# Performance work log

Measured on AMD Instinct MI355X. Metric: run time of the kernel, lower is better.

The kernel has to match this reference:

```python
import math
import jax, jax.numpy as jnp
import numpy as np

B, S, H = 4, 4096, 1024
NH, HD = 16, 64
MLP_DIM = 4096


def _gelu_tanh(x):
    c = math.sqrt(2.0 / math.pi)
    return 0.5 * x * (1.0 + jnp.tanh(c * (x + 0.044715 * x * x * x)))


def _layernorm(x, w, b, eps=1e-5):
    mu = jnp.mean(x, axis=-1, keepdims=True)
    var = jnp.var(x, axis=-1, keepdims=True)
    return (x - mu) * jax.lax.rsqrt(var + eps) * w + b


def setup_inputs() -> dict:
    key = jax.random.key(0)
    ks = jax.random.split(key, 12)
    s = 0.02
    return {
        "x": jax.random.normal(ks[0], (B, S, H), jnp.float32),
        "ln1_w": jnp.ones((H,), jnp.float32),
        "ln1_b": jnp.zeros((H,), jnp.float32),
        "q_w": jax.random.normal(ks[1], (H, H), jnp.float32) * s,
        "q_b": jnp.zeros((H,), jnp.float32),
        "k_w": jax.random.normal(ks[2], (H, H), jnp.float32) * s,
        "k_b": jnp.zeros((H,), jnp.float32),
        "v_w": jax.random.normal(ks[3], (H, H), jnp.float32) * s,
        "v_b": jnp.zeros((H,), jnp.float32),
        "o_w": jax.random.normal(ks[4], (H, H), jnp.float32) * s,
        "o_b": jnp.zeros((H,), jnp.float32),
        "ln2_w": jnp.ones((H,), jnp.float32),
        "ln2_b": jnp.zeros((H,), jnp.float32),
        "fc_w": jax.random.normal(ks[5], (H, MLP_DIM), jnp.float32) * s,
        "fc_b": jnp.zeros((MLP_DIM,), jnp.float32),
        "proj_w": jax.random.normal(ks[6], (MLP_DIM, H), jnp.float32) * (s / math.sqrt(2 * 12)),
        "proj_b": jnp.zeros((H,), jnp.float32),
    }


def reference(x, ln1_w, ln1_b, q_w, q_b, k_w, k_b, v_w, v_b, o_w, o_b,
              ln2_w, ln2_b, fc_w, fc_b, proj_w, proj_b):
    bsz, seqlen, h = x.shape
    ln_x = _layernorm(x, ln1_w, ln1_b)

    # projections -> [b, nh, t, hd]
    def heads(y):
        return y.reshape(bsz, seqlen, NH, HD).transpose(0, 2, 1, 3)

    q = heads(ln_x @ q_w + q_b)
    k = heads(ln_x @ k_w + k_b)
    v = heads(ln_x @ v_w + v_b)

    # feature map: elu(x)+1
    qf = jax.nn.elu(q) + 1.0
    kf = jax.nn.elu(k) + 1.0

    kv = jnp.einsum('bhtd,bhte->bhde', kf, v)              # [b,nh,hd,hd]
    norm = 1.0 / (jnp.einsum('bhtd,bhd->bht', qf, kf.sum(axis=2)) + 1e-6)
    out = jnp.einsum('bhtd,bhde->bhte', qf, kv) * norm[..., None]
    out = out.transpose(0, 2, 1, 3).reshape(bsz, seqlen, h)
    attn = out @ o_w + o_b

    x = x + attn
    h_mlp = _gelu_tanh(_layernorm(x, ln2_w, ln2_b) @ fc_w + fc_b)
    x = x + (h_mlp @ proj_w + proj_b)
    return x
```

## Files before the change

### kernel.cpp

```cpp
#include <hip/hip_runtime.h>
#include <hip/hip_bf16.h>
#include <cstdint>
#include <cstddef>

typedef __bf16 bf16;
typedef __bf16 bf16x8 __attribute__((ext_vector_type(8)));
typedef __bf16 bf16x4 __attribute__((ext_vector_type(4)));
typedef float  f32x4  __attribute__((ext_vector_type(4)));

typedef __attribute__((address_space(1))) void gvoid_t;
typedef __attribute__((address_space(3))) void lvoid_t;

#define GLD_LDS16(g, l) __builtin_amdgcn_global_load_lds( \
    (gvoid_t*)(uintptr_t)(g), (lvoid_t*)(uint32_t)(uintptr_t)(l), 16, 0, 0)

#define SBAR() __builtin_amdgcn_s_barrier()
#define SCHED_FENCE() __builtin_amdgcn_sched_barrier(0)
#define WAIT_VMN(n) asm volatile("s_waitcnt vmcnt(" #n ")" ::: "memory")
#define WAIT_LGKM0() asm volatile("s_waitcnt lgkmcnt(0)" ::: "memory")

__global__ __launch_bounds__(256) void transpose4(
    const float* __restrict__ qw, const float* __restrict__ kw,
    const float* __restrict__ vw, const float* __restrict__ ow,
    bf16* __restrict__ wqkvT, bf16* __restrict__ woT)
{
  __shared__ float tile[32][33];
  const int z = blockIdx.z;
  const float* in = z == 0 ? qw : (z == 1 ? kw : (z == 2 ? vw : ow));
  bf16* out = z == 3 ? woT : (wqkvT + (size_t)z * 1024 * 1024);
  const int bx = blockIdx.x, by = blockIdx.y;
  const int tx = threadIdx.x, ty = threadIdx.y;
#pragma unroll
  for (int i = 0; i < 32; i += 8)
    tile[ty + i][tx] = in[(size_t)(by * 32 + ty + i) * 1024 + bx * 32 + tx];
  __syncthreads();
#pragma unroll
  for (int i = 0; i < 32; i += 8)
    out[(size_t)(bx * 32 + ty + i) * 1024 + by * 32 + tx] = (bf16)tile[tx][ty + i];
}

__global__ __launch_bounds__(256) void transpose_cast(
    const float* __restrict__ in, bf16* __restrict__ out, int R, int C)
{
  __shared__ float tile[32][33];
  const int bx = blockIdx.x, by = blockIdx.y;
  const int tx = threadIdx.x, ty = threadIdx.y;
#pragma unroll
  for (int i = 0; i < 32; i += 8)
    tile[ty + i][tx] = in[(size_t)(by * 32 + ty + i) * C + bx * 32 + tx];
  __syncthreads();
#pragma unroll
  for (int i = 0; i < 32; i += 8)
    out[(size_t)(bx * 32 + ty + i) * R + by * 32 + tx] = (bf16)tile[tx][ty + i];
}

__global__ __launch_bounds__(256) void pack3(
    const float* __restrict__ a, const float* __restrict__ b,
    const float* __restrict__ c, float* __restrict__ o)
{
  const int i = blockIdx.x * 256 + threadIdx.x;
  o[i] = i < 1024 ? a[i] : (i < 2048 ? b[i - 1024] : c[i - 2048]);
}

__global__ __launch_bounds__(256) void ln_row(
    const float* __restrict__ x, const float* __restrict__ w,
    const float* __restrict__ b, bf16* __restrict__ out)
{
  const int row = blockIdx.x;
  const int tid = threadIdx.x;
  const float4 v = ((const float4*)(x + (size_t)row * 1024))[tid];
  float s  = v.x + v.y + v.z + v.w;
  float ss = v.x * v.x + v.y * v.y + v.z * v.z + v.w * v.w;
#pragma unroll
  for (int off = 32; off > 0; off >>= 1) {
    s  += __shfl_down(s, off);
    ss += __shfl_down(ss, off);
  }
  __shared__ float red[8];
  const int wid = tid >> 6, lane = tid & 63;
  if (lane == 0) { red[wid] = s; red[4 + wid] = ss; }
  __syncthreads();
  s  = red[0] + red[1] + red[2] + red[3];
  ss = red[4] + red[5] + red[6] + red[7];
  const float mu   = s * (1.f / 1024.f);
  const float var  = ss * (1.f / 1024.f) - mu * mu;
  const float rstd = rsqrtf(var + 1e-5f);
  const float4 wv = ((const float4*)w)[tid];
  const float4 bv = ((const float4*)b)[tid];
  bf16x4 ov;
  ov[0] = (bf16)((v.x - mu) * rstd * wv.x + bv.x);
  ov[1] = (bf16)((v.y - mu) * rstd * wv.y + bv.y);
  ov[2] = (bf16)((v.z - mu) * rstd * wv.z + bv.z);
  ov[3] = (bf16)((v.w - mu) * rstd * wv.w + bv.w);
  *(bf16x4*)(out + (size_t)row * 1024 + tid * 4) = ov;
}

template <int EPI>
__global__ __launch_bounds__(512, 2) void gemm256(
    const bf16* __restrict__ A, const bf16* __restrict__ BT,
    const float* __restrict__ bias, const float* __restrict__ resid,
    void* __restrict__ outp, int M, int N, int K, int nx)
{
  __shared__ __align__(16) char lds[131072];
  const int tid  = threadIdx.x;
  const int wid  = tid >> 6, lane = tid & 63;
  const int wr   = wid >> 2, wc = wid & 3;
  const int ln15 = lane & 15, lhi = lane >> 4;

  const int nwg = (int)gridDim.x;
  const int cpx = nwg >> 3;
  const int bid = (int)blockIdx.x;
  const int lg  = (bid & 7) * cpx + (bid >> 3);
  const int bx  = lg % nx, by = lg / nx;
  const int row0 = by << 8, col0 = bx << 8;

  const int srowA = tid >> 3;
  const int sslA  = (tid & 7) ^ (srowA & 7);
  const bf16* aS  = A + (size_t)(row0 + srowA) * K + sslA * 8;
  const size_t rjK = (size_t)K << 6;
  const int u8    = tid >> 3, s8 = tid & 7;
  const int gRowB = ((u8 >> 5) << 6) + (u8 & 31);
  const int sslB  = s8 ^ (u8 & 7);
  const bf16* bS  = BT + (size_t)(col0 + gRowB) * K + sslB * 8;

  char* ldsAw = lds + wid * 1024;
  char* ldsBw = lds + 65536 + wid * 1024;

  const int slk0 = (lhi ^ (ln15 & 7)) << 4;
  const int slk1 = ((4 + lhi) ^ (ln15 & 7)) << 4;
  const int rowA0 = ((wr << 7) + ln15) * 128;
  const int rowB0 = 65536 + (wc * 32 + ln15) * 128;

  f32x4 acc[8][4] = {};
  bf16x8 a[4][2], b0[2][2], b1[2][2];
  const int nt = K >> 6;

#define STG_A(D, KT, I) GLD_LDS16(aS + (size_t)(I) * rjK + (size_t)(KT) * 64, \
                                  ldsAw + (D) * 32768 + (I) * 8192)
#define STG_B(D, KT, NH, J) GLD_LDS16(bS + (size_t)((J) * 128 + (NH) * 32) * K + (size_t)(KT) * 64, \
                                      ldsBw + (D) * 32768 + (NH) * 16384 + (J) * 8192)
#define RD_A(D, MH) do { _Pragma("unroll") \
    for (int m_ = 0; m_ < 4; ++m_) { \
      a[m_][0] = *(const bf16x8*)(lds + (D) * 32768 + rowA0 + (MH) * 8192 + m_ * 2048 + slk0); \
      a[m_][1] = *(const bf16x8*)(lds + (D) * 32768 + rowA0 + (MH) * 8192 + m_ * 2048 + slk1); \
    } } while (0)
#define RD_B(D, NH, DST) do { _Pragma("unroll") \
    for (int n_ = 0; n_ < 2; ++n_) { \
      DST[n_][0] = *(const bf16x8*)(lds + (D) * 32768 + rowB0 + (NH) * 16384 + n_ * 2048 + slk0); \
      DST[n_][1] = *(const bf16x8*)(lds + (D) * 32768 + rowB0 + (NH) * 16384 + n_ * 2048 + slk1); \
    } } while (0)
#define MFMA8(MH, NH, BSRC) do { \
    __builtin_amdgcn_s_setprio(1); \
    _Pragma("unroll") for (int m_ = 0; m_ < 4; ++m_) \
    _Pragma("unroll") for (int n_ = 0; n_ < 2; ++n_) { \
      acc[(MH) * 4 + m_][(NH) * 2 + n_] = __builtin_amdgcn_mfma_f32_16x16x32_bf16( \
          a[m_][0], BSRC[n_][0], acc[(MH) * 4 + m_][(NH) * 2 + n_], 0, 0, 0); \
      acc[(MH) * 4 + m_][(NH) * 2 + n_] = __builtin_amdgcn_mfma_f32_16x16x32_bf16( \
          a[m_][1], BSRC[n_][1], acc[(MH) * 4 + m_][(NH) * 2 + n_], 0, 0, 0); \
    } \
    __builtin_amdgcn_s_setprio(0); } while (0)

  STG_A(0, 0, 0); STG_A(0, 0, 2);
  STG_B(0, 0, 0, 0); STG_B(0, 0, 0, 1);
  STG_B(0, 0, 1, 0); STG_B(0, 0, 1, 1);
  STG_A(0, 0, 1); STG_A(0, 0, 3);
  WAIT_VMN(0);
  SBAR(); SCHED_FENCE();

  for (int kt = 0; kt < nt - 1; ++kt) {
    const int d = kt & 1, dn = d ^ 1;
    RD_A(d, 0); RD_B(d, 0, b0);
    STG_A(dn, kt + 1, 0); STG_A(dn, kt + 1, 2);
    SBAR(); WAIT_LGKM0(); SCHED_FENCE();
    MFMA8(0, 0, b0);
    SBAR(); SCHED_FENCE();
    RD_B(d, 1, b1);
    STG_B(dn, kt + 1, 0, 0); STG_B(dn, kt + 1, 0, 1);
    WAIT_VMN(4);
    SBAR(); WAIT_LGKM0(); SCHED_FENCE();
    MFMA8(0, 1, b1);
    SBAR(); SCHED_FENCE();
    RD_A(d, 1);
    STG_B(dn, kt + 1, 1, 0); STG_B(dn, kt + 1, 1, 1);
    SBAR(); WAIT_LGKM0(); SCHED_FENCE();
    MFMA8(1, 0, b0);
    SBAR(); SCHED_FENCE();
    STG_A(dn, kt + 1, 1); STG_A(dn, kt + 1, 3);
    MFMA8(1, 1, b1);
    WAIT_VMN(2);
    SBAR(); SCHED_FENCE();
  }

  {
    const int d = (nt - 1) & 1;
    RD_A(d, 0); RD_B(d, 0, b0);
    SBAR(); WAIT_LGKM0(); SCHED_FENCE();
    MFMA8(0, 0, b0);
    SBAR(); SCHED_FENCE();
    RD_B(d, 1, b1);
    WAIT_VMN(0);
    SBAR(); WAIT_LGKM0(); SCHED_FENCE();
    MFMA8(0, 1, b1);
    SBAR(); SCHED_FENCE();
    RD_A(d, 1);
    WAIT_LGKM0(); SCHED_FENCE();
    MFMA8(1, 0, b0);
    MFMA8(1, 1, b1);
  }
#undef STG_A
#undef STG_B
#undef RD_A
#undef RD_B
#undef MFMA8

  const int lr4 = lhi << 2;
#pragma unroll
  for (int m = 0; m < 8; ++m) {
#pragma unroll
    for (int n = 0; n < 4; ++n) {
      const int c_i = col0 + wc * 64 + n * 16 + ln15;
      const float bv = bias[c_i];
#pragma unroll
      for (int j = 0; j < 4; ++j) {
        const int r_i = row0 + wr * 128 + m * 16 + lr4 + j;
        const size_t idx = (size_t)r_i * N + c_i;
        float val = acc[m][n][j] + bv;
        if constexpr (EPI == 0) {
          ((bf16*)outp)[idx] = (bf16)val;
        } else if constexpr (EPI == 1) {
          ((bf16*)outp)[idx] = (bf16)(val > 0.f ? val + 1.f : __expf(val));
        } else if constexpr (EPI == 2) {
          ((float*)outp)[idx] = val + resid[idx];
        } else if constexpr (EPI == 3) {
          const float u  = 0.7978845608028654f * (val + 0.044715f * val * val * val);
          const float th = 1.f - 2.f / (__expf(2.f * u) + 1.f);
          ((bf16*)outp)[idx] = (bf16)(0.5f * val * (1.f + th));
        } else {
          if (c_i < 2048)
            ((bf16*)outp)[idx] = (bf16)(val > 0.f ? val + 1.f : __expf(val));
          else
            ((bf16*)outp)[idx] = (bf16)val;
        }
      }
    }
  }
}

__global__ __launch_bounds__(256) void kv_part_kernel(
    const bf16* __restrict__ qkv, float* __restrict__ kv_part,
    float* __restrict__ ksum_part)
{
  const int bh = blockIdx.x >> 3, ch = blockIdx.x & 7;
  const int b = bh >> 4, h = bh & 15;
  const int tid = threadIdx.x;
  const int d = tid & 63, eg = tid >> 6;
  const size_t grow0 = (size_t)b * 4096 + (size_t)ch * 512;
  const size_t vbase = 2048 + (size_t)h * 64;
  __shared__ bf16 svv[8][64], skf[8][64];
  float accum[16];
#pragma unroll
  for (int i = 0; i < 16; ++i) accum[i] = 0.f;
  float ks = 0.f;
  const int tt = tid >> 5, cc = (tid & 31) << 1;
  for (int t0 = 0; t0 < 512; t0 += 8) {
    __syncthreads();
    const size_t base = (grow0 + t0 + tt) * 3072 + vbase + cc;
    *(uint32_t*)&svv[tt][cc] = *(const uint32_t*)(qkv + base);
    *(uint32_t*)&skf[tt][cc] = *(const uint32_t*)(qkv + base - 1024);
    __syncthreads();
#pragma unroll
    for (int q = 0; q < 8; ++q) {
      const float kd = (float)skf[q][d];
      const uint32_t* u0 = (const uint32_t*)&svv[q][eg * 16];
#pragma unroll
      for (int i = 0; i < 8; ++i) {
        const uint32_t u = u0[i];
        const float lo = __uint_as_float(u << 16);
        const float hi = __uint_as_float(u & 0xffff0000u);
        accum[2 * i]     += lo * kd;
        accum[2 * i + 1] += hi * kd;
      }
    }
    if (tid < 64) {
#pragma unroll
      for (int q = 0; q < 8; ++q) ks += (float)skf[q][tid];
    }
  }
  float* op = kv_part + (size_t)blockIdx.x * 4096 + (size_t)(eg * 16) * 64 + d;
#pragma unroll
  for (int ee = 0; ee < 16; ++ee) op[ee * 64] = accum[ee];
  if (tid < 64) ksum_part[(size_t)blockIdx.x * 64 + tid] = ks;
}

__global__ __launch_bounds__(256) void kv_reduce(
    const float* __restrict__ kvp, const float* __restrict__ ksp,
    bf16* __restrict__ kb)
{
  const int bh = blockIdx.x;
  const int tid = threadIdx.x;
  bf16* KB = kb + (size_t)bh * 5120;
  for (int i = tid; i < 4096; i += 256) {
    float s = 0.f;
#pragma unroll
    for (int ch = 0; ch < 8; ++ch) s += kvp[((size_t)bh * 8 + ch) * 4096 + i];
    KB[i] = (bf16)s;
  }
  if (tid < 64) {
    float s = 0.f;
#pragma unroll
    for (int ch = 0; ch < 8; ++ch) s += ksp[((size_t)bh * 8 + ch) * 64 + tid];
    KB[4096 + tid] = (bf16)s;
  }
  for (int i = 4160 + tid; i < 5120; i += 256) KB[i] = (bf16)0.f;
}

__global__ __launch_bounds__(256) void attn_mfma(
    const bf16* __restrict__ qkv, const bf16* __restrict__ kb,
    bf16* __restrict__ attn)
{
  const int bh = blockIdx.x >> 4, rb = blockIdx.x & 15;
  const int b = bh >> 4, h = bh & 15;
  const int tid = threadIdx.x, wid = tid >> 6, lane = tid & 63;
  const int ln15 = lane & 15, lhi = lane >> 4;
  const size_t row0 = (size_t)b * 4096 + rb * 256 + wid * 64;
  const bf16* KB = kb + (size_t)bh * 5120;

  bf16x8 bfr[5][2];
#pragma unroll
  for (int nb = 0; nb < 5; ++nb)
#pragma unroll
    for (int ks = 0; ks < 2; ++ks)
      bfr[nb][ks] = *(const bf16x8*)(KB + (nb * 16 + ln15) * 64 + ks * 32 + lhi * 8);

  for (int mt = 0; mt < 4; ++mt) {
    const bf16* ap = qkv + (row0 + mt * 16 + ln15) * 3072 + h * 64 + lhi * 8;
    const bf16x8 a0 = *(const bf16x8*)ap;
    const bf16x8 a1 = *(const bf16x8*)(ap + 32);
    f32x4 acc[5];
#pragma unroll
    for (int nb = 0; nb < 5; ++nb) {
      f32x4 z = {0.f, 0.f, 0.f, 0.f};
      z = __builtin_amdgcn_mfma_f32_16x16x32_bf16(a0, bfr[nb][0], z, 0, 0, 0);
      acc[nb] = __builtin_amdgcn_mfma_f32_16x16x32_bf16(a1, bfr[nb][1], z, 0, 0, 0);
    }
#pragma unroll
    for (int j = 0; j < 4; ++j) {
      const float ns = __shfl(acc[4][j], (lane & 48));
      const float inv = 1.f / (ns + 1e-6f);
      const size_t r = row0 + mt * 16 + (lhi << 2) + j;
#pragma unroll
      for (int nb = 0; nb < 4; ++nb)
        attn[r * 1024 + h * 64 + nb * 16 + ln15] = (bf16)(acc[nb][j] * inv);
    }
  }
}

extern "C" void kernel_launch(void* const* d_in, const int* in_sizes, int n_in,
                              void* d_out, int out_size, void* d_ws, size_t ws_size,
                              hipStream_t stream)
{
  const float* x    = (const float*)d_in[0];
  const float* ln1w = (const float*)d_in[1];
  const float* ln1b = (const float*)d_in[2];
  const float* qw   = (const float*)d_in[3];
  const float* qb   = (const float*)d_in[4];
  const float* kw   = (const float*)d_in[5];
  const float* kb_  = (const float*)d_in[6];
  const float* vw   = (const float*)d_in[7];
  const float* vb   = (const float*)d_in[8];
  const float* ow   = (const float*)d_in[9];
  const float* ob   = (const float*)d_in[10];
  const float* ln2w = (const float*)d_in[11];
  const float* ln2b = (const float*)d_in[12];
  const float* fcw  = (const float*)d_in[13];
  const float* fcb  = (const float*)d_in[14];
  const float* pjw  = (const float*)d_in[15];
  const float* pjb  = (const float*)d_in[16];
  float* out = (float*)d_out;
  char* ws = (char*)d_ws;

  constexpr size_t O_LNX  = 0;
  constexpr size_t O_QKV  = 33554432;
  constexpr size_t O_HMLP = 0;
  constexpr size_t O_KVP  = 134217728;
  constexpr size_t O_KSP  = 142606336;
  constexpr size_t O_KB   = 142737408;
  constexpr size_t O_ATTN = 143802368;
  constexpr size_t O_LN2  = 177356800;
  constexpr size_t O_WQ   = 210911232;
  constexpr size_t O_WO   = 217202688;
  constexpr size_t O_WFC  = 219299840;
  constexpr size_t O_WPJ  = 227688448;

  bf16* lnx   = (bf16*)(ws + O_LNX);
  bf16* qkv   = (bf16*)(ws + O_QKV);
  bf16* hmlp  = (bf16*)(ws + O_HMLP);
  float* kvp  = (float*)(ws + O_KVP);
  float* qkvb = (float*)(ws + O_KVP);
  float* ksp  = (float*)(ws + O_KSP);
  bf16* kbt   = (bf16*)(ws + O_KB);
  bf16* attn  = (bf16*)(ws + O_ATTN);
  bf16* ln2h  = (bf16*)(ws + O_LN2);
  bf16* wqkvT = (bf16*)(ws + O_WQ);
  bf16* woT   = (bf16*)(ws + O_WO);
  bf16* wfcT  = (bf16*)(ws + O_WFC);
  bf16* wpjT  = (bf16*)(ws + O_WPJ);

  const dim3 tb(32, 8);
  transpose4<<<dim3(32, 32, 4), tb, 0, stream>>>(qw, kw, vw, ow, wqkvT, woT);
  transpose_cast<<<dim3(128, 32), tb, 0, stream>>>(fcw, wfcT, 1024, 4096);
  transpose_cast<<<dim3(32, 128), tb, 0, stream>>>(pjw, wpjT, 4096, 1024);
  pack3<<<12, 256, 0, stream>>>(qb, kb_, vb, qkvb);

  ln_row<<<16384, 256, 0, stream>>>(x, ln1w, ln1b, lnx);

  gemm256<4><<<768, 512, 0, stream>>>(lnx, wqkvT, qkvb, nullptr, qkv, 16384, 3072, 1024, 12);

  kv_part_kernel<<<512, 256, 0, stream>>>(qkv, kvp, ksp);
  kv_reduce<<<64, 256, 0, stream>>>(kvp, ksp, kbt);
  attn_mfma<<<1024, 256, 0, stream>>>(qkv, kbt, attn);

  gemm256<2><<<256, 512, 0, stream>>>(attn, woT, ob, x, out, 16384, 1024, 1024, 4);

  ln_row<<<16384, 256, 0, stream>>>(out, ln2w, ln2b, ln2h);

  gemm256<3><<<1024, 512, 0, stream>>>(ln2h, wfcT, fcb, nullptr, hmlp, 16384, 4096, 1024, 16);

  gemm256<2><<<256, 512, 0, stream>>>(hmlp, wpjT, pjb, out, out, 16384, 1024, 4096, 4);
}
```

Before: 606.3 us.

## Run MLP GEMMs in FP8 with scaled weights and FP8 activations

Converts the fc and proj weights to FP8 e4m3 with a fixed scale of 4, makes the second layernorm and the GELU epilogue emit FP8, and adds a new FP8 MFMA GEMM kernel that uses 64-byte K tiles and less LDS. This halves operand bytes and uses the higher-throughput FP8 matrix instructions for the two largest GEMMs. The cost is much lower precision for activations and weights, using a hand-written software FP8 conversion, which risks going past the accuracy tolerance.

```diff
diff --git a/kernel.cpp b/kernel.cpp
--- a/kernel.cpp
+++ b/kernel.cpp
@@ -18,6 +18,36 @@
 #define SCHED_FENCE() __builtin_amdgcn_sched_barrier(0)
 #define WAIT_VMN(n) asm volatile("s_waitcnt vmcnt(" #n ")" ::: "memory")
 #define WAIT_LGKM0() asm volatile("s_waitcnt lgkmcnt(0)" ::: "memory")
+
+__device__ inline uint8_t to_fp8(float x)
+{
+  uint32_t u = __float_as_uint(x);
+  const uint8_t s = (u >> 24) & 0x80u;
+  const int e = (int)((u >> 23) & 0xff) - 127;
+  const uint32_t m = u & 0x7fffffu;
+  if (((u >> 23) & 0xff) == 0xff) return s | 0x7e;
+  if (e > 8 || (e == 8 && m > 0x600000u)) return s | 0x7e;
+  if (e >= -6) {
+    uint32_t mant = m >> 20;
+    const uint32_t rest = m & 0xfffffu;
+    const uint32_t rnd = (rest > 0x80000u) || (rest == 0x80000u && (mant & 1));
+    mant += rnd;
+    uint32_t ee = (uint32_t)(e + 7);
+    if (mant == 8) { mant = 0; ee += 1; }
+    if (ee > 15 || (ee == 15 && mant > 6)) return s | 0x7e;
+    return s | (ee << 3) | mant;
+  }
+  if (e < -10) return s;
+  const int sh = 20 + (-6 - e);
+  const uint32_t sig = 0x800000u | m;
+  uint32_t mant = sig >> sh;
+  const uint32_t rem = sig & ((1u << sh) - 1u);
+  const uint32_t half = 1u << (sh - 1);
+  const uint32_t rnd = (rem > half) || (rem == half && (mant & 1));
+  mant += rnd;
+  if (mant >= 8) return s | (1u << 3);
+  return s | mant;
+}
 
 __global__ __launch_bounds__(256) void transpose4(
     const float* __restrict__ qw, const float* __restrict__ kw,
@@ -39,8 +69,9 @@
     out[(size_t)(bx * 32 + ty + i) * 1024 + by * 32 + tx] = (bf16)tile[tx][ty + i];
 }
 
-__global__ __launch_bounds__(256) void transpose_cast(
-    const float* __restrict__ in, bf16* __restrict__ out, int R, int C)
+__global__ __launch_bounds__(256) void transpose_cast_f8(
+    const float* __restrict__ in, uint8_t* __restrict__ out, int R, int C,
+    float scale)
 {
   __shared__ float tile[32][33];
   const int bx = blockIdx.x, by = blockIdx.y;
@@ -51,7 +82,7 @@
   __syncthreads();
 #pragma unroll
   for (int i = 0; i < 32; i += 8)
-    out[(size_t)(bx * 32 + ty + i) * R + by * 32 + tx] = (bf16)tile[tx][ty + i];
+    out[(size_t)(bx * 32 + ty + i) * R + by * 32 + tx] = to_fp8(tile[tx][ty + i] * scale);
 }
 
 __global__ __launch_bounds__(256) void pack3(
@@ -62,9 +93,10 @@
   o[i] = i < 1024 ? a[i] : (i < 2048 ? b[i - 1024] : c[i - 2048]);
 }
 
+template <int OUT8>
 __global__ __launch_bounds__(256) void ln_row(
     const float* __restrict__ x, const float* __restrict__ w,
-    const float* __restrict__ b, bf16* __restrict__ out)
+    const float* __restrict__ b, void* __restrict__ outp)
 {
   const int row = blockIdx.x;
   const int tid = threadIdx.x;
@@ -87,12 +119,19 @@
   const float rstd = rsqrtf(var + 1e-5f);
   const float4 wv = ((const float4*)w)[tid];
   const float4 bv = ((const float4*)b)[tid];
-  bf16x4 ov;
-  ov[0] = (bf16)((v.x - mu) * rstd * wv.x + bv.x);
-  ov[1] = (bf16)((v.y - mu) * rstd * wv.y + bv.y);
-  ov[2] = (bf16)((v.z - mu) * rstd * wv.z + bv.z);
-  ov[3] = (bf16)((v.w - mu) * rstd * wv.w + bv.w);
-  *(bf16x4*)(out + (size_t)row * 1024 + tid * 4) = ov;
+  float o0 = (v.x - mu) * rstd * wv.x + bv.x;
+  float o1 = (v.y - mu) * rstd * wv.y + bv.y;
+  float o2 = (v.z - mu) * rstd * wv.z + bv.z;
+  float o3 = (v.w - mu) * rstd * wv.w + bv.w;
+  if constexpr (OUT8) {
+    uint8_t* out = (uint8_t*)outp;
+    const size_t base = (size_t)row * 1024 + tid * 4;
+    uchar4 q = {to_fp8(o0), to_fp8(o1), to_fp8(o2), to_fp8(o3)};
+    *(uchar4*)(out + base) = q;
+  } else {
+    bf16x4 ov; ov[0] = (bf16)o0; ov[1] = (bf16)o1; ov[2] = (bf16)o2; ov[3] = (bf16)o3;
+    *(bf16x4*)((bf16*)outp + (size_t)row * 1024 + tid * 4) = ov;
+  }
 }
 
 template <int EPI>
@@ -231,15 +270,118 @@
           ((bf16*)outp)[idx] = (bf16)(val > 0.f ? val + 1.f : __expf(val));
         } else if constexpr (EPI == 2) {
           ((float*)outp)[idx] = val + resid[idx];
-        } else if constexpr (EPI == 3) {
-          const float u  = 0.7978845608028654f * (val + 0.044715f * val * val * val);
-          const float th = 1.f - 2.f / (__expf(2.f * u) + 1.f);
-          ((bf16*)outp)[idx] = (bf16)(0.5f * val * (1.f + th));
         } else {
           if (c_i < 2048)
             ((bf16*)outp)[idx] = (bf16)(val > 0.f ? val + 1.f : __expf(val));
           else
             ((bf16*)outp)[idx] = (bf16)val;
+        }
+      }
+    }
+  }
+}
+
+template <int EPI>
+__global__ __launch_bounds__(512, 2) void gemm256f8(
+    const uint8_t* __restrict__ A, const uint8_t* __restrict__ BT,
+    const float* __restrict__ bias, const float* __restrict__ resid,
+    void* __restrict__ outp, int M, int N, int K, int nx)
+{
+  __shared__ __align__(16) char lds[65536];
+  const int tid  = threadIdx.x;
+  const int wid  = tid >> 6, lane = tid & 63;
+  const int wr   = wid >> 2, wc = wid & 3;
+  const int ln15 = lane & 15, lhi = lane >> 4;
+
+  const int nwg = (int)gridDim.x;
+  const int cpx = nwg >> 3;
+  const int bid = (int)blockIdx.x;
+  const int lg  = (bid & 7) * cpx + (bid >> 3);
+  const int bx  = lg % nx, by = lg / nx;
+  const int row0 = by << 8, col0 = bx << 8;
+
+  const int srow  = tid >> 2;
+  const int sslot = (tid & 3) ^ (srow & 3);
+  const uint8_t* aS = A  + (size_t)(row0 + srow) * K + sslot * 16;
+  const uint8_t* bS = BT + (size_t)(col0 + srow) * K + sslot * 16;
+  const size_t rjump = (size_t)K << 7;
+  char* ldsW = lds + wid * 1024;
+
+  const int sub  = (lhi & 1) * 8;
+  const int g0   = lhi >> 1;
+  const int slkK0 = ((g0) ^ (ln15 & 3)) * 16 + sub;
+  const int slkK1 = ((2 + g0) ^ (ln15 & 3)) * 16 + sub;
+  const int rowA0 = (wr * 128 + ln15) * 64;
+  const int rowB0 = 32768 + (wc * 64 + ln15) * 64;
+
+  f32x4 acc[8][4] = {};
+  const int nt = K >> 6;
+
+#define STG8(D, KT) do { \
+    const uint8_t* ga_ = aS + (size_t)(KT) * 64; \
+    const uint8_t* gb_ = bS + (size_t)(KT) * 64; \
+    char* la_ = ldsW + (D) * 16384; \
+    GLD_LDS16(ga_,         la_); \
+    GLD_LDS16(ga_ + rjump, la_ + 8192); \
+    GLD_LDS16(gb_,         la_ + 32768); \
+    GLD_LDS16(gb_ + rjump, la_ + 40960); \
+  } while (0)
+
+  STG8(0, 0);
+  WAIT_VMN(0);
+  SBAR();
+
+  for (int kt = 0; kt < nt; ++kt) {
+    const int d = kt & 1;
+    const char* base = (const char*)lds + d * 16384;
+    if (kt + 1 < nt) STG8(d ^ 1, kt + 1);
+
+    long a0v[8], b0v[4], a1v[8], b1v[4];
+#pragma unroll
+    for (int m = 0; m < 8; ++m) a0v[m] = *(const long*)(base + rowA0 + m * 1024 + slkK0);
+#pragma unroll
+    for (int n = 0; n < 4; ++n) b0v[n] = *(const long*)(base + rowB0 + n * 1024 + slkK0);
+#pragma unroll
+    for (int m = 0; m < 8; ++m) a1v[m] = *(const long*)(base + rowA0 + m * 1024 + slkK1);
+#pragma unroll
+    for (int n = 0; n < 4; ++n) b1v[n] = *(const long*)(base + rowB0 + n * 1024 + slkK1);
+
+    __builtin_amdgcn_s_setprio(1);
+#pragma unroll
+    for (int m = 0; m < 8; ++m)
+#pragma unroll
+      for (int n = 0; n < 4; ++n)
+        acc[m][n] = __builtin_amdgcn_mfma_f32_16x16x32_fp8_fp8(a0v[m], b0v[n], acc[m][n], 0, 0, 0);
+#pragma unroll
+    for (int m = 0; m < 8; ++m)
+#pragma unroll
+      for (int n = 0; n < 4; ++n)
+        acc[m][n] = __builtin_amdgcn_mfma_f32_16x16x32_fp8_fp8(a1v[m], b1v[n], acc[m][n], 0, 0, 0);
+    __builtin_amdgcn_s_setprio(0);
+
+    WAIT_VMN(0);
+    SBAR();
+  }
+#undef STG8
+
+  const int lr4 = lhi << 2;
+#pragma unroll
+  for (int m = 0; m < 8; ++m) {
+#pragma unroll
+    for (int n = 0; n < 4; ++n) {
+      const int c_i = col0 + wc * 64 + n * 16 + ln15;
+      const float bv = bias[c_i];
+#pragma unroll
+      for (int j = 0; j < 4; ++j) {
+        const int r_i = row0 + wr * 128 + m * 16 + lr4 + j;
+        const size_t idx = (size_t)r_i * N + c_i;
+        float val = acc[m][n][j] * 0.25f + bv;
+        if constexpr (EPI == 2) {
+          ((float*)outp)[idx] = val + resid[idx];
+        } else {
+          const float u  = 0.7978845608028654f * (val + 0.044715f * val * val * val);
+          const float th = 1.f - 2.f / (__expf(2.f * u) + 1.f);
+          ((uint8_t*)outp)[idx] = to_fp8(0.5f * val * (1.f + th));
         }
       }
     }
@@ -392,27 +534,27 @@
   constexpr size_t O_WFC  = 219299840;
   constexpr size_t O_WPJ  = 227688448;
 
-  bf16* lnx   = (bf16*)(ws + O_LNX);
-  bf16* qkv   = (bf16*)(ws + O_QKV);
-  bf16* hmlp  = (bf16*)(ws + O_HMLP);
-  float* kvp  = (float*)(ws + O_KVP);
-  float* qkvb = (float*)(ws + O_KVP);
-  float* ksp  = (float*)(ws + O_KSP);
-  bf16* kbt   = (bf16*)(ws + O_KB);
-  bf16* attn  = (bf16*)(ws + O_ATTN);
-  bf16* ln2h  = (bf16*)(ws + O_LN2);
-  bf16* wqkvT = (bf16*)(ws + O_WQ);
-  bf16* woT   = (bf16*)(ws + O_WO);
-  bf16* wfcT  = (bf16*)(ws + O_WFC);
-  bf16* wpjT  = (bf16*)(ws + O_WPJ);
+  bf16* lnx    = (bf16*)(ws + O_LNX);
+  bf16* qkv    = (bf16*)(ws + O_QKV);
+  uint8_t* hmlp8 = (uint8_t*)(ws + O_HMLP);
+  float* kvp   = (float*)(ws + O_KVP);
+  float* qkvb  = (float*)(ws + O_KVP);
+  float* ksp   = (float*)(ws + O_KSP);
+  bf16* kbt    = (bf16*)(ws + O_KB);
+  bf16* attn   = (bf16*)(ws + O_ATTN);
+  uint8_t* ln2h8 = (uint8_t*)(ws + O_LN2);
+  bf16* wqkvT  = (bf16*)(ws + O_WQ);
+  bf16* woT    = (bf16*)(ws + O_WO);
+  uint8_t* wfc8 = (uint8_t*)(ws + O_WFC);
+  uint8_t* wpj8 = (uint8_t*)(ws + O_WPJ);
 
   const dim3 tb(32, 8);
   transpose4<<<dim3(32, 32, 4), tb, 0, stream>>>(qw, kw, vw, ow, wqkvT, woT);
-  transpose_cast<<<dim3(128, 32), tb, 0, stream>>>(fcw, wfcT, 1024, 4096);
-  transpose_cast<<<dim3(32, 128), tb, 0, stream>>>(pjw, wpjT, 4096, 1024);
+  transpose_cast_f8<<<dim3(128, 32), tb, 0, stream>>>(fcw, wfc8, 1024, 4096, 4.f);
+  transpose_cast_f8<<<dim3(32, 128), tb, 0, stream>>>(pjw, wpj8, 4096, 1024, 4.f);
   pack3<<<12, 256, 0, stream>>>(qb, kb_, vb, qkvb);
 
-  ln_row<<<16384, 256, 0, stream>>>(x, ln1w, ln1b, lnx);
+  ln_row<0><<<16384, 256, 0, stream>>>(x, ln1w, ln1b, lnx);
 
   gemm256<4><<<768, 512, 0, stream>>>(lnx, wqkvT, qkvb, nullptr, qkv, 16384, 3072, 1024, 12);
 
@@ -422,9 +564,9 @@
 
   gemm256<2><<<256, 512, 0, stream>>>(attn, woT, ob, x, out, 16384, 1024, 1024, 4);
 
-  ln_row<<<16384, 256, 0, stream>>>(out, ln2w, ln2b, ln2h);
-
-  gemm256<3><<<1024, 512, 0, stream>>>(ln2h, wfcT, fcb, nullptr, hmlp, 16384, 4096, 1024, 16);
-
-  gemm256<2><<<256, 512, 0, stream>>>(hmlp, wpjT, pjb, out, out, 16384, 1024, 4096, 4);
-}
+  ln_row<1><<<16384, 256, 0, stream>>>(out, ln2w, ln2b, ln2h8);
+
+  gemm256f8<3><<<1024, 512, 0, stream>>>(ln2h8, wfc8, fcb, nullptr, hmlp8, 16384, 4096, 1024, 16);
+
+  gemm256f8<2><<<256, 512, 0, stream>>>(hmlp8, wpj8, pjb, out, out, 16384, 1024, 4096, 4);
+}
```

Measured after the change: 813.6 us. 34.2% more time.
